# Kernel optimization log

Hardware: AMD Instinct MI355X
Metric: run time of the kernel (lower is better)

## Reference

```python
import jax, jax.numpy as jnp
import numpy as np

L, B, C, H = 1024, 8, 1024, 16
D = C // H  # 64


def setup_inputs() -> dict:
    key = jax.random.key(0)
    ks = jax.random.split(key, 8)
    hidden_states = jax.random.normal(ks[0], (L, B, C), dtype=jnp.float32)
    rotary_pos_emb = jax.random.uniform(ks[1], (L, D // 2), dtype=jnp.float32) * 10.0
    attention_mask = jax.random.randint(ks[2], (B, L, L), 0, 2) > 0
    s = 1.0 / np.sqrt(C)
    Wqkv = jax.random.uniform(ks[3], (3 * C, C), dtype=jnp.float32, minval=-s, maxval=s)
    bqkv = jax.random.uniform(ks[4], (3 * C,), dtype=jnp.float32, minval=-s, maxval=s)
    Wo = jax.random.uniform(ks[5], (C, C), dtype=jnp.float32, minval=-s, maxval=s)
    bo = jax.random.uniform(ks[6], (C,), dtype=jnp.float32, minval=-s, maxval=s)
    return {"hidden_states": hidden_states, "rotary_pos_emb": rotary_pos_emb,
            "attention_mask": attention_mask, "Wqkv": Wqkv, "bqkv": bqkv, "Wo": Wo, "bo": bo}


def _rotate_half(x):
    # interleaved pairs: [-x1, x0, -x3, x2, ...]
    x2 = x.reshape(*x.shape[:-1], -1, 2)
    return jnp.stack((-x2[..., 1], x2[..., 0]), axis=-1).reshape(x.shape)


def reference(hidden_states, rotary_pos_emb, attention_mask, Wqkv, bqkv, Wo, bo):
    Lx, Bx, Cx = hidden_states.shape
    # QKV projection: (L,B,3C) -> (3,B,L,H,D)
    qkv = hidden_states @ Wqkv.T + bqkv
    qkv = qkv.reshape(Lx, Bx, 3, H, D).transpose(2, 1, 0, 3, 4)
    q, k, v = qkv[0], qkv[1], qkv[2]  # (B, L, H, D)
    # RoPE: freqs (L, D/2) -> cos/sin (1, L, 1, D) via duplication
    rpe = rotary_pos_emb[None] if rotary_pos_emb.ndim == 2 else rotary_pos_emb
    cos = jnp.concatenate([jnp.cos(rpe), jnp.cos(rpe)], axis=-1)[:, :, None, :]
    sin = jnp.concatenate([jnp.sin(rpe), jnp.sin(rpe)], axis=-1)[:, :, None, :]
    q = q * cos + _rotate_half(q) * sin
    k = k * cos + _rotate_half(k) * sin
    # (B, H, L, D)
    q = q.transpose(0, 2, 1, 3)
    k = k.transpose(0, 2, 1, 3)
    v = v.transpose(0, 2, 1, 3)
    scale = 1.0 / jnp.sqrt(jnp.asarray(D, dtype=q.dtype))
    scores = jnp.einsum('bhqd,bhkd->bhqk', q, k) * scale
    # torch SDPA bool mask: True = attend, False = masked
    scores = jnp.where(attention_mask[:, None, :, :], scores, jnp.finfo(scores.dtype).min)
    attn = jax.nn.softmax(scores, axis=-1)
    out = jnp.einsum('bhqk,bhkd->bhqd', attn, v)  # (B, H, L, D)
    out = out.transpose(2, 0, 1, 3).reshape(Lx, Bx, Cx)  # (L, B, C)
    return out @ Wo.T + bo
```

## Files before the change

kernel.cpp:

```cpp
#include <hip/hip_runtime.h>
#include <hip/hip_bf16.h>

typedef short bf16x8 __attribute__((ext_vector_type(8)));
typedef short bf16x4 __attribute__((ext_vector_type(4)));
typedef float f32x4 __attribute__((ext_vector_type(4)));
typedef unsigned int u32;
typedef unsigned long long u64;

#define GLD_LDS16(gp, lp) \
  __builtin_amdgcn_global_load_lds((const __attribute__((address_space(1))) u32*)(gp), \
                                   (__attribute__((address_space(3))) u32*)(lp), 16, 0, 0)

__device__ __forceinline__ short f2bf(float f) {
  u32 u = __builtin_bit_cast(u32, f);
  u = (u + 0x7fffu + ((u >> 16) & 1u)) >> 16;
  return (short)u;
}

__device__ __forceinline__ u32 pack2_bf16(float a, float b) {
#if __has_builtin(__builtin_amdgcn_cvt_pk_bf16_f32)
  typedef __bf16 bf16v2 __attribute__((ext_vector_type(2)));
  bf16v2 r = __builtin_amdgcn_cvt_pk_bf16_f32(a, b);
  return __builtin_bit_cast(u32, r);
#else
  return (u32)(unsigned short)f2bf(a) | ((u32)(unsigned short)f2bf(b) << 16);
#endif
}

__device__ __forceinline__ float exp2_fast(float x) {
#if __has_builtin(__builtin_amdgcn_exp2f)
  return __builtin_amdgcn_exp2f(x);
#else
  return exp2f(x);
#endif
}

__device__ __forceinline__ f32x4 mfma_16x16x16_bf16(bf16x4 a, bf16x4 b, f32x4 c) {
#if __has_builtin(__builtin_amdgcn_mfma_f32_16x16x16_bf16)
  return __builtin_amdgcn_mfma_f32_16x16x16_bf16(a, b, c, 0, 0, 0);
#elif __has_builtin(__builtin_amdgcn_mfma_f32_16x16x16bf16_1k)
  return __builtin_amdgcn_mfma_f32_16x16x16bf16_1k(a, b, c, 0, 0, 0);
#else
  f32x4 d = c;
  __asm__ volatile("v_mfma_f32_16x16x16_bf16 %0, %1, %2, %0\n\ts_nop 7\n\ts_nop 7"
                   : "+v"(d) : "v"(a), "v"(b));
  return d;
#endif
}


__global__ void cvt_f32_bf16(const float* __restrict__ in, short* __restrict__ out, int n4) {
  int i = (blockIdx.x * 256 + threadIdx.x) * 4;
  float4 v = *(const float4*)(in + i);
  short4 o;
  o.x = f2bf(v.x); o.y = f2bf(v.y); o.z = f2bf(v.z); o.w = f2bf(v.w);
  *(short4*)(out + i) = o;
}

__global__ void rope_tables(const float* __restrict__ rpe, float* __restrict__ cosT,
                            float* __restrict__ sinT) {
  int i = blockIdx.x * 256 + threadIdx.x;
  float v = rpe[i];
  cosT[i] = cosf(v);
  sinT[i] = sinf(v);
}

__global__ void mask_pack(const int* __restrict__ m, u64* __restrict__ out) {
  int i = blockIdx.x * 256 + threadIdx.x;
  u64 bm = __ballot(m[i] != 0);
  if ((threadIdx.x & 63) == 0) out[i >> 6] = bm;
}

__global__ __launch_bounds__(256, 2) void gemm_qkv(
    const short* __restrict__ Xb, const short* __restrict__ Wb,
    const float* __restrict__ bqkv, const float* __restrict__ cosT,
    const float* __restrict__ sinT, short* __restrict__ qb,
    short* __restrict__ kbuf, short* __restrict__ vbuf) {
  __shared__ short Ash[128 * 32];
  __shared__ short Bsh[128 * 32];
  const int tid = threadIdx.x;
  const int wid = tid >> 6, lane = tid & 63;
  const int g = lane >> 4, c = lane & 15;
  const int wm = wid >> 1, wn = wid & 1;
  const int m0 = blockIdx.y * 128, n0 = blockIdx.x * 128;

  f32x4 acc[4][4];
  for (int i = 0; i < 4; i++)
    for (int j = 0; j < 4; j++) acc[i][j] = (f32x4){0.f, 0.f, 0.f, 0.f};

  const int srow = lane >> 2;
  const int scol = (lane & 3) * 8;
  const short* AgL = Xb + (long)(m0 + wid * 32 + srow) * 1024 + scol;
  const short* BgL = Wb + (long)(n0 + wid * 32 + srow) * 1024 + scol;
  short* As0 = &Ash[(wid * 32) * 32];
  short* As1 = &Ash[(wid * 32 + 16) * 32];
  short* Bs0 = &Bsh[(wid * 32) * 32];
  short* Bs1 = &Bsh[(wid * 32 + 16) * 32];

  for (int kt = 0; kt < 32; ++kt) {
    const int ko = kt * 32;
    GLD_LDS16(AgL + ko, As0);
    GLD_LDS16(AgL + ko + 16 * 1024, As1);
    GLD_LDS16(BgL + ko, Bs0);
    GLD_LDS16(BgL + ko + 16 * 1024, Bs1);
    __syncthreads();
    bf16x8 af[4], bfr[4];
    for (int i = 0; i < 4; i++)
      af[i] = *(const bf16x8*)&Ash[(wm * 64 + i * 16 + c) * 32 + g * 8];
    for (int j = 0; j < 4; j++)
      bfr[j] = *(const bf16x8*)&Bsh[(wn * 64 + j * 16 + c) * 32 + g * 8];
    for (int i = 0; i < 4; i++)
      for (int j = 0; j < 4; j++)
        acc[i][j] = __builtin_amdgcn_mfma_f32_16x16x32_bf16(bfr[j], af[i], acc[i][j], 0, 0, 0);
    __syncthreads();
  }

  for (int jt = 0; jt < 4; jt++) {
    const int chan = n0 + wn * 64 + jt * 16 + g * 4;
    const int three = chan >> 10;
    const int hh = (chan >> 6) & 15;
    const int d = chan & 63;
    const float4 bq = *(const float4*)&bqkv[chan];
    for (int i = 0; i < 4; i++) {
      const int r = m0 + wm * 64 + i * 16 + c;
      const int l = r >> 3, b = r & 7;
      float v0 = acc[i][jt][0] + bq.x;
      float v1 = acc[i][jt][1] + bq.y;
      float v2 = acc[i][jt][2] + bq.z;
      float v3 = acc[i][jt][3] + bq.w;
      const long doff = ((long)(b * 16 + hh) * 1024 + l) * 64 + d;
      if (three == 2) {
        uint2 o = {pack2_bf16(v0, v1), pack2_bf16(v2, v3)};
        *(uint2*)&vbuf[doff] = o;
      } else {
        const float4 cs = *(const float4*)&cosT[l * 32 + (d & 31)];
        const float4 sn = *(const float4*)&sinT[l * 32 + (d & 31)];
        float e0 = v0 * cs.x - v1 * sn.x;
        float o0 = v1 * cs.y + v0 * sn.y;
        float e1 = v2 * cs.z - v3 * sn.z;
        float o1 = v3 * cs.w + v2 * sn.w;
        short* dst;
        if (three == 0) {
          const float S = 0.18033688011f;
          e0 *= S; o0 *= S; e1 *= S; o1 *= S;
          dst = qb;
        } else {
          dst = kbuf;
        }
        uint2 o = {pack2_bf16(e0, o0), pack2_bf16(e1, o1)};
        *(uint2*)&dst[doff] = o;
      }
    }
  }
}

__global__ __launch_bounds__(256) void transpose_v(const short* __restrict__ vbuf,
                                                   short* __restrict__ vTb) {
  __shared__ short T[64 * 72];
  const int bh = blockIdx.y;
  const int l0 = blockIdx.x * 64;
  const int t = threadIdx.x;
  const int row = t >> 3;
  const int cc = (t & 7) * 8;
  const short* src = vbuf + ((long)bh * 1024 + l0) * 64;
  for (int p = 0; p < 2; p++) {
    int lr = row + p * 32;
    *(bf16x8*)&T[lr * 72 + cc] = *(const bf16x8*)&src[(long)lr * 64 + cc];
  }
  __syncthreads();
  short* dst = vTb + (long)bh * 64 * 1024 + l0;
  for (int p = 0; p < 2; p++) {
    int d = row + p * 32;
    bf16x8 v;
    for (int j = 0; j < 8; j++) v[j] = T[(cc + j) * 72 + d];
    *(bf16x8*)&dst[(long)d * 1024 + cc] = v;
  }
}

__global__ __launch_bounds__(256, 5) void flash_attn(
    const short* __restrict__ qb, const short* __restrict__ kbuf,
    const short* __restrict__ vTb, const u64* __restrict__ maskb,
    short* __restrict__ attno) {
  __shared__ short K0[64 * 64], K1[64 * 64];
  __shared__ short V0[64 * 64], V1[64 * 64];
  const int t = threadIdx.x;
  const int wid = t >> 6, lane = t & 63;
  const int g = lane >> 4, c = lane & 15;
  const int q0 = blockIdx.x * 64;
  const int bh = blockIdx.y;
  const int b = bh >> 4;
  const int h = bh & 15;
  const long qoff = (long)bh * 1024 * 64;
  const int qrow = q0 + wid * 16 + c;

  bf16x8 aq0, aq1;
  {
    const short* qp = qb + qoff + (long)qrow * 64;
    aq0 = *(const bf16x8*)(qp + g * 8);
    aq1 = *(const bf16x8*)(qp + 32 + g * 8);
  }

  f32x4 Od[4];
  for (int i = 0; i < 4; i++) Od[i] = (f32x4){0.f, 0.f, 0.f, 0.f};
  f32x4 Ld = (f32x4){0.f, 0.f, 0.f, 0.f};
  float m_run = -1e30f;

  bf16x4 avOnes;
  {
    union { bf16x4 v; u32 u[2]; } av;
    av.u[0] = av.u[1] = (c == 0) ? 0x3F803F80u : 0u;
    avOnes = av.v;
  }

  const u64* mrow = maskb + ((long)b * 1024 + qrow) * 16;
  const short* Kg = kbuf + qoff;
  const short* Vg = vTb + qoff;

  const int l8 = lane >> 3, l7 = lane & 7;
  const int sr = wid * 16 + l8;
  const int sch = ((l7 ^ l8) & 7) * 8;

  const int ck0 = g ^ (c & 7);
  const int kOff0 = c * 64 + ck0 * 8;
  const int kOff1 = c * 64 + (ck0 ^ 4) * 8;
  int vOff[4];
  for (int nt = 0; nt < 4; nt++)
    vOff[nt] = c * 64 + (((2 * nt + (g >> 1)) ^ (c & 7)) * 8) + (g & 1) * 4;

#define STAGE(KD, VD, ktn) do { \
    GLD_LDS16(Kg + (long)((ktn) + sr) * 64 + sch,       &KD[(wid * 16) * 64]); \
    GLD_LDS16(Kg + (long)((ktn) + sr + 8) * 64 + sch,   &KD[(wid * 16 + 8) * 64]); \
    GLD_LDS16(Vg + (long)sr * 1024 + (ktn) + sch,       &VD[(wid * 16) * 64]); \
    GLD_LDS16(Vg + (long)(sr + 8) * 1024 + (ktn) + sch, &VD[(wid * 16 + 8) * 64]); \
  } while (0)

#define TILE(KB, VB, KP, VP, ki) do { \
    u64 mw = mrow[ki];  \
    __syncthreads();  \
    STAGE(KP, VP, (((ki) + 1) & 15) * 64); \
    f32x4 z[4]; \
    for (int nt = 0; nt < 4; nt++) { \
      bf16x8 bk0 = *(const bf16x8*)&KB[kOff0 + nt * 1024]; \
      bf16x8 bk1 = *(const bf16x8*)&KB[kOff1 + nt * 1024]; \
      f32x4 zz = (f32x4){0.f, 0.f, 0.f, 0.f}; \
      zz = __builtin_amdgcn_mfma_f32_16x16x32_bf16(bk0, aq0, zz, 0, 0, 0); \
      zz = __builtin_amdgcn_mfma_f32_16x16x32_bf16(bk1, aq1, zz, 0, 0, 0); \
      z[nt] = zz; \
    } \
    float mx = fmaxf(fmaxf(z[0][0], z[0][1]), fmaxf(z[0][2], z[0][3])); \
    for (int nt = 1; nt < 4; nt++) \
      mx = fmaxf(mx, fmaxf(fmaxf(z[nt][0], z[nt][1]), fmaxf(z[nt][2], z[nt][3]))); \
    mx = fmaxf(mx, __shfl_xor(mx, 16, 64)); \
    mx = fmaxf(mx, __shfl_xor(mx, 32, 64)); \
    float mnew = fmaxf(m_run, mx); \
    if (__ballot(mnew > m_run)) { \
      float al = exp2_fast(m_run - mnew); \
      for (int dt = 0; dt < 4; dt++) { \
        Od[dt][0] *= al; Od[dt][1] *= al; Od[dt][2] *= al; Od[dt][3] *= al; \
      } \
      Ld[0] *= al; \
      m_run = mnew; \
    } \
    bf16x4 pb[4]; \
    for (int nt = 0; nt < 4; nt++) { \
      u32 m4 = (u32)(mw >> (nt * 16 + g * 4)) & 0xFu; \
      u32 mlo = ((m4 & 1u) ? 0xFFFFu : 0u) | ((m4 & 2u) ? 0xFFFF0000u : 0u); \
      u32 mhi = ((m4 & 4u) ? 0xFFFFu : 0u) | ((m4 & 8u) ? 0xFFFF0000u : 0u); \
      float p0 = exp2_fast(z[nt][0] - mnew); \
      float p1 = exp2_fast(z[nt][1] - mnew); \
      float p2 = exp2_fast(z[nt][2] - mnew); \
      float p3 = exp2_fast(z[nt][3] - mnew); \
      union { bf16x4 v; u32 u[2]; } pu; \
      pu.u[0] = pack2_bf16(p0, p1) & mlo; \
      pu.u[1] = pack2_bf16(p2, p3) & mhi; \
      pb[nt] = pu.v; \
    } \
    for (int nt = 0; nt < 4; nt++) { \
      Ld = mfma_16x16x16_bf16(avOnes, pb[nt], Ld); \
      for (int dt = 0; dt < 4; dt++) { \
        bf16x4 av = *(const bf16x4*)&VB[vOff[nt] + dt * 1024]; \
        Od[dt] = mfma_16x16x16_bf16(av, pb[nt], Od[dt]); \
      } \
    } \
  } while (0)

  STAGE(K0, V0, 0);
  for (int ki = 0; ki < 16; ki += 2) {
    TILE(K0, V0, K1, V1, ki);
    TILE(K1, V1, K0, V0, ki + 1);
  }
#undef TILE
#undef STAGE

  float lsum = __shfl(Ld[0], c, 64);
  float inv = 1.f / lsum;
  long rbase = ((long)qrow * 8 + b) * 1024 + h * 64 + g * 4;
  for (int dt = 0; dt < 4; dt++) {
    union { bf16x4 v; u32 u[2]; } o;
    o.u[0] = pack2_bf16(Od[dt][0] * inv, Od[dt][1] * inv);
    o.u[1] = pack2_bf16(Od[dt][2] * inv, Od[dt][3] * inv);
    *(bf16x4*)&attno[rbase + dt * 16] = o.v;
  }
}

__global__ __launch_bounds__(256, 2) void gemm_out(
    const short* __restrict__ Ab, const short* __restrict__ Wob,
    const float* __restrict__ bo, float* __restrict__ out) {
  __shared__ short Ash[128 * 32];
  __shared__ short Bsh[128 * 32];
  const int tid = threadIdx.x;
  const int wid = tid >> 6, lane = tid & 63;
  const int g = lane >> 4, c = lane & 15;
  const int wm = wid >> 1, wn = wid & 1;
  const int m0 = blockIdx.y * 128, n0 = blockIdx.x * 128;

  f32x4 acc[4][4];
  for (int i = 0; i < 4; i++)
    for (int j = 0; j < 4; j++) acc[i][j] = (f32x4){0.f, 0.f, 0.f, 0.f};

  const int srow = lane >> 2;
  const int scol = (lane & 3) * 8;
  const short* AgL = Ab + (long)(m0 + wid * 32 + srow) * 1024 + scol;
  const short* BgL = Wob + (long)(n0 + wid * 32 + srow) * 1024 + scol;
  short* As0 = &Ash[(wid * 32) * 32];
  short* As1 = &Ash[(wid * 32 + 16) * 32];
  short* Bs0 = &Bsh[(wid * 32) * 32];
  short* Bs1 = &Bsh[(wid * 32 + 16) * 32];

  for (int kt = 0; kt < 32; ++kt) {
    const int ko = kt * 32;
    GLD_LDS16(AgL + ko, As0);
    GLD_LDS16(AgL + ko + 16 * 1024, As1);
    GLD_LDS16(BgL + ko, Bs0);
    GLD_LDS16(BgL + ko + 16 * 1024, Bs1);
    __syncthreads();
    bf16x8 af[4], bfr[4];
    for (int i = 0; i < 4; i++)
      af[i] = *(const bf16x8*)&Ash[(wm * 64 + i * 16 + c) * 32 + g * 8];
    for (int j = 0; j < 4; j++)
      bfr[j] = *(const bf16x8*)&Bsh[(wn * 64 + j * 16 + c) * 32 + g * 8];
    for (int i = 0; i < 4; i++)
      for (int j = 0; j < 4; j++)
        acc[i][j] = __builtin_amdgcn_mfma_f32_16x16x32_bf16(af[i], bfr[j], acc[i][j], 0, 0, 0);
    __syncthreads();
  }

  for (int jt = 0; jt < 4; jt++) {
    const int j = n0 + wn * 64 + jt * 16 + c;
    const float bias = bo[j];
    for (int i = 0; i < 4; i++) {
      const int rbase = m0 + wm * 64 + i * 16 + g * 4;
      for (int reg = 0; reg < 4; reg++)
        out[(long)(rbase + reg) * 1024 + j] = acc[i][jt][reg] + bias;
    }
  }
}

extern "C" void kernel_launch(void* const* d_in, const int* in_sizes, int n_in,
                              void* d_out, int out_size, void* d_ws, size_t ws_size,
                              hipStream_t stream) {
  const float* hs = (const float*)d_in[0];
  const float* rpe = (const float*)d_in[1];
  const int* amask = (const int*)d_in[2];
  const float* Wqkv = (const float*)d_in[3];
  const float* bqkv = (const float*)d_in[4];
  const float* Wo = (const float*)d_in[5];
  const float* bo = (const float*)d_in[6];
  float* out = (float*)d_out;

  char* ws = (char*)d_ws;
  auto alloc = [&](size_t bytes) {
    char* p = ws;
    ws += (bytes + 255) & ~(size_t)255;
    return p;
  };
  short* Xb = (short*)alloc(8192LL * 1024 * 2);
  short* Wqkvb = (short*)alloc(3072LL * 1024 * 2);
  short* Wob = (short*)alloc(1024LL * 1024 * 2);
  float* cosT = (float*)alloc(1024 * 32 * 4);
  float* sinT = (float*)alloc(1024 * 32 * 4);
  u64* maskb = (u64*)alloc(8LL * 1024 * 16 * 8);
  short* qb = (short*)alloc(128LL * 1024 * 64 * 2);
  short* kbuf = (short*)alloc(128LL * 1024 * 64 * 2);
  short* vbuf = (short*)alloc(128LL * 1024 * 64 * 2);
  short* vTb = (short*)alloc(128LL * 1024 * 64 * 2);
  short* attno = (short*)alloc(8192LL * 1024 * 2);

  cvt_f32_bf16<<<8192 * 1024 / 4 / 256, 256, 0, stream>>>(hs, Xb, 8192 * 1024);
  cvt_f32_bf16<<<3072 * 1024 / 4 / 256, 256, 0, stream>>>(Wqkv, Wqkvb, 3072 * 1024);
  cvt_f32_bf16<<<1024 * 1024 / 4 / 256, 256, 0, stream>>>(Wo, Wob, 1024 * 1024);
  rope_tables<<<128, 256, 0, stream>>>(rpe, cosT, sinT);
  mask_pack<<<32768, 256, 0, stream>>>(amask, maskb);
  gemm_qkv<<<dim3(24, 64), 256, 0, stream>>>(Xb, Wqkvb, bqkv, cosT, sinT, qb, kbuf, vbuf);
  transpose_v<<<dim3(16, 128), 256, 0, stream>>>(vbuf, vTb);
  flash_attn<<<dim3(16, 128), 256, 0, stream>>>(qb, kbuf, vTb, maskb, attno);
  gemm_out<<<dim3(8, 64), 256, 0, stream>>>(attno, Wob, bo, out);
}
```

Baseline: 345.3 us.

## Use 16x16x32 MFMA for PV, lazy softmax rescale, fuse bf16 conversion kernels

The PV and row-sum products now use the 16x16x32 bf16 MFMA instead of 16x16x16. This halves the number of MFMA instructions and makes the V loads 8-wide. To match that operand layout, K rows are permuted when staged into LDS. The running max is only updated, with its cross-lane shuffles, when some lane's max exceeds the current one by more than 8 (in log2 units). This skips most rescales but lets exponentials grow up to 2^8 before renormalising. The three f32-to-bf16 conversion launches are merged into one kernel, and the pack helper gains an inline-asm fallback.

New measurement: 329.1 us. -4.7%, faster.

```diff
diff --git a/kernel.cpp b/kernel.cpp
--- a/kernel.cpp
+++ b/kernel.cpp
@@ -23,7 +23,9 @@
   bf16v2 r = __builtin_amdgcn_cvt_pk_bf16_f32(a, b);
   return __builtin_bit_cast(u32, r);
 #else
-  return (u32)(unsigned short)f2bf(a) | ((u32)(unsigned short)f2bf(b) << 16);
+  u32 r;
+  asm("v_cvt_pk_bf16_f32 %0, %1, %2" : "=v"(r) : "v"(a), "v"(b));
+  return r;
 #endif
 }
 
@@ -35,22 +37,23 @@
 #endif
 }
 
-__device__ __forceinline__ f32x4 mfma_16x16x16_bf16(bf16x4 a, bf16x4 b, f32x4 c) {
-#if __has_builtin(__builtin_amdgcn_mfma_f32_16x16x16_bf16)
-  return __builtin_amdgcn_mfma_f32_16x16x16_bf16(a, b, c, 0, 0, 0);
-#elif __has_builtin(__builtin_amdgcn_mfma_f32_16x16x16bf16_1k)
-  return __builtin_amdgcn_mfma_f32_16x16x16bf16_1k(a, b, c, 0, 0, 0);
-#else
-  f32x4 d = c;
-  __asm__ volatile("v_mfma_f32_16x16x16_bf16 %0, %1, %2, %0\n\ts_nop 7\n\ts_nop 7"
-                   : "+v"(d) : "v"(a), "v"(b));
-  return d;
-#endif
-}
-
-
-__global__ void cvt_f32_bf16(const float* __restrict__ in, short* __restrict__ out, int n4) {
-  int i = (blockIdx.x * 256 + threadIdx.x) * 4;
+
+__global__ __launch_bounds__(256) void cvt_all(
+    const float* __restrict__ hs, const float* __restrict__ wqkv,
+    const float* __restrict__ wo, short* __restrict__ xb,
+    short* __restrict__ wqkvb, short* __restrict__ wob) {
+  int b = blockIdx.x;
+  const float* in;
+  short* out;
+  int base;
+  if (b < 8192) {
+    in = hs; out = xb; base = b * 1024;
+  } else if (b < 8192 + 3072) {
+    in = wqkv; out = wqkvb; base = (b - 8192) * 1024;
+  } else {
+    in = wo; out = wob; base = (b - 11264) * 1024;
+  }
+  int i = base + threadIdx.x * 4;
   float4 v = *(const float4*)(in + i);
   short4 o;
   o.x = f2bf(v.x); o.y = f2bf(v.y); o.z = f2bf(v.z); o.w = f2bf(v.w);
@@ -205,11 +208,12 @@
   f32x4 Ld = (f32x4){0.f, 0.f, 0.f, 0.f};
   float m_run = -1e30f;
 
-  bf16x4 avOnes;
+  bf16x8 avOnes8;
   {
-    union { bf16x4 v; u32 u[2]; } av;
-    av.u[0] = av.u[1] = (c == 0) ? 0x3F803F80u : 0u;
-    avOnes = av.v;
+    union { bf16x8 v; u32 u[4]; } av;
+    u32 o1 = (c == 0) ? 0x3F803F80u : 0u;
+    av.u[0] = av.u[1] = av.u[2] = av.u[3] = o1;
+    avOnes8 = av.v;
   }
 
   const u64* mrow = maskb + ((long)b * 1024 + qrow) * 16;
@@ -219,17 +223,21 @@
   const int l8 = lane >> 3, l7 = lane & 7;
   const int sr = wid * 16 + l8;
   const int sch = ((l7 ^ l8) & 7) * 8;
+  const int r1 = wid * 16 + l8;
+  const int r2 = r1 + 8;
+  const int kp1 = (r1 & 32) | (((r1 & 15) >> 2) << 3) | (((r1 >> 4) & 1) << 2) | (r1 & 3);
+  const int kp2 = (r2 & 32) | (((r2 & 15) >> 2) << 3) | (((r2 >> 4) & 1) << 2) | (r2 & 3);
 
   const int ck0 = g ^ (c & 7);
   const int kOff0 = c * 64 + ck0 * 8;
   const int kOff1 = c * 64 + (ck0 ^ 4) * 8;
-  int vOff[4];
-  for (int nt = 0; nt < 4; nt++)
-    vOff[nt] = c * 64 + (((2 * nt + (g >> 1)) ^ (c & 7)) * 8) + (g & 1) * 4;
+  int vOff32[2];
+  for (int kg = 0; kg < 2; kg++)
+    vOff32[kg] = c * 64 + (((kg * 4 + g) ^ (c & 7)) * 8);
 
 #define STAGE(KD, VD, ktn) do { \
-    GLD_LDS16(Kg + (long)((ktn) + sr) * 64 + sch,       &KD[(wid * 16) * 64]); \
-    GLD_LDS16(Kg + (long)((ktn) + sr + 8) * 64 + sch,   &KD[(wid * 16 + 8) * 64]); \
+    GLD_LDS16(Kg + (long)((ktn) + kp1) * 64 + sch,      &KD[(wid * 16) * 64]); \
+    GLD_LDS16(Kg + (long)((ktn) + kp2) * 64 + sch,      &KD[(wid * 16 + 8) * 64]); \
     GLD_LDS16(Vg + (long)sr * 1024 + (ktn) + sch,       &VD[(wid * 16) * 64]); \
     GLD_LDS16(Vg + (long)(sr + 8) * 1024 + (ktn) + sch, &VD[(wid * 16 + 8) * 64]); \
   } while (0)
@@ -247,13 +255,14 @@
       zz = __builtin_amdgcn_mfma_f32_16x16x32_bf16(bk1, aq1, zz, 0, 0, 0); \
       z[nt] = zz; \
     } \
-    float mx = fmaxf(fmaxf(z[0][0], z[0][1]), fmaxf(z[0][2], z[0][3])); \
-    for (int nt = 1; nt < 4; nt++) \
-      mx = fmaxf(mx, fmaxf(fmaxf(z[nt][0], z[nt][1]), fmaxf(z[nt][2], z[nt][3]))); \
-    mx = fmaxf(mx, __shfl_xor(mx, 16, 64)); \
-    mx = fmaxf(mx, __shfl_xor(mx, 32, 64)); \
-    float mnew = fmaxf(m_run, mx); \
-    if (__ballot(mnew > m_run)) { \
+    float mx = fmaxf(fmaxf(fmaxf(z[0][0], z[0][1]), fmaxf(z[0][2], z[0][3])), \
+                     fmaxf(fmaxf(z[1][0], z[1][1]), fmaxf(z[1][2], z[1][3]))); \
+    mx = fmaxf(mx, fmaxf(fmaxf(fmaxf(z[2][0], z[2][1]), fmaxf(z[2][2], z[2][3])), \
+                         fmaxf(fmaxf(z[3][0], z[3][1]), fmaxf(z[3][2], z[3][3])))); \
+    if (__ballot(mx > m_run + 8.f)) {  \
+      mx = fmaxf(mx, __shfl_xor(mx, 16, 64)); \
+      mx = fmaxf(mx, __shfl_xor(mx, 32, 64)); \
+      float mnew = fmaxf(m_run, mx); \
       float al = exp2_fast(m_run - mnew); \
       for (int dt = 0; dt < 4; dt++) { \
         Od[dt][0] *= al; Od[dt][1] *= al; Od[dt][2] *= al; Od[dt][3] *= al; \
@@ -261,25 +270,24 @@
       Ld[0] *= al; \
       m_run = mnew; \
     } \
-    bf16x4 pb[4]; \
-    for (int nt = 0; nt < 4; nt++) { \
-      u32 m4 = (u32)(mw >> (nt * 16 + g * 4)) & 0xFu; \
-      u32 mlo = ((m4 & 1u) ? 0xFFFFu : 0u) | ((m4 & 2u) ? 0xFFFF0000u : 0u); \
-      u32 mhi = ((m4 & 4u) ? 0xFFFFu : 0u) | ((m4 & 8u) ? 0xFFFF0000u : 0u); \
-      float p0 = exp2_fast(z[nt][0] - mnew); \
-      float p1 = exp2_fast(z[nt][1] - mnew); \
-      float p2 = exp2_fast(z[nt][2] - mnew); \
-      float p3 = exp2_fast(z[nt][3] - mnew); \
-      union { bf16x4 v; u32 u[2]; } pu; \
-      pu.u[0] = pack2_bf16(p0, p1) & mlo; \
-      pu.u[1] = pack2_bf16(p2, p3) & mhi; \
-      pb[nt] = pu.v; \
-    } \
-    for (int nt = 0; nt < 4; nt++) { \
-      Ld = mfma_16x16x16_bf16(avOnes, pb[nt], Ld); \
+    for (int kg = 0; kg < 2; kg++) { \
+      union { bf16x8 v; u32 u[4]; } pu; \
+      for (int ntp = 0; ntp < 2; ntp++) { \
+        const int nt = kg * 2 + ntp; \
+        u32 m4 = (u32)(mw >> (kg * 32 + g * 8 + ntp * 4)) & 0xFu; \
+        u32 mlo = ((m4 & 1u) ? 0xFFFFu : 0u) | ((m4 & 2u) ? 0xFFFF0000u : 0u); \
+        u32 mhi = ((m4 & 4u) ? 0xFFFFu : 0u) | ((m4 & 8u) ? 0xFFFF0000u : 0u); \
+        float p0 = exp2_fast(z[nt][0] - m_run); \
+        float p1 = exp2_fast(z[nt][1] - m_run); \
+        float p2 = exp2_fast(z[nt][2] - m_run); \
+        float p3 = exp2_fast(z[nt][3] - m_run); \
+        pu.u[ntp * 2 + 0] = pack2_bf16(p0, p1) & mlo; \
+        pu.u[ntp * 2 + 1] = pack2_bf16(p2, p3) & mhi; \
+      } \
+      Ld = __builtin_amdgcn_mfma_f32_16x16x32_bf16(avOnes8, pu.v, Ld, 0, 0, 0); \
       for (int dt = 0; dt < 4; dt++) { \
-        bf16x4 av = *(const bf16x4*)&VB[vOff[nt] + dt * 1024]; \
-        Od[dt] = mfma_16x16x16_bf16(av, pb[nt], Od[dt]); \
+        bf16x8 av = *(const bf16x8*)&VB[vOff32[kg] + dt * 1024]; \
+        Od[dt] = __builtin_amdgcn_mfma_f32_16x16x32_bf16(av, pu.v, Od[dt], 0, 0, 0); \
       } \
     } \
   } while (0)
@@ -386,9 +394,7 @@
   short* vTb = (short*)alloc(128LL * 1024 * 64 * 2);
   short* attno = (short*)alloc(8192LL * 1024 * 2);
 
-  cvt_f32_bf16<<<8192 * 1024 / 4 / 256, 256, 0, stream>>>(hs, Xb, 8192 * 1024);
-  cvt_f32_bf16<<<3072 * 1024 / 4 / 256, 256, 0, stream>>>(Wqkv, Wqkvb, 3072 * 1024);
-  cvt_f32_bf16<<<1024 * 1024 / 4 / 256, 256, 0, stream>>>(Wo, Wob, 1024 * 1024);
+  cvt_all<<<12288, 256, 0, stream>>>(hs, Wqkv, Wo, Xb, Wqkvb, Wob);
   rope_tables<<<128, 256, 0, stream>>>(rpe, cosT, sinT);
   mask_pack<<<32768, 256, 0, stream>>>(amask, maskb);
   gemm_qkv<<<dim3(24, 64), 256, 0, stream>>>(Xb, Wqkvb, bqkv, cosT, sinT, qb, kbuf, vbuf);
```
